# Kernel tuning notes

Measured on AMD Instinct MI355X. Metric: run time of the kernel, lower is better.

## Reference

```python
import jax, jax.numpy as jnp
import numpy as np

N = 50000
E = 800000
F_IN = 128
HID = 128
N_CLS = 32


def setup_inputs() -> dict:
    key = jax.random.key(0)
    ks = jax.random.split(key, 8)
    x = jax.random.normal(ks[0], (N, F_IN), dtype=jnp.float32)
    edge_index = jax.random.randint(ks[1], (2, E), 0, N, dtype=jnp.int32)
    batch = jnp.zeros((N,), dtype=jnp.int32)
    # GCNConv learned params (glorot-ish scale)
    W1 = jax.random.normal(ks[2], (F_IN, HID), dtype=jnp.float32) / np.sqrt(F_IN)
    b1 = jnp.zeros((HID,), dtype=jnp.float32)
    W2 = jax.random.normal(ks[3], (HID, HID), dtype=jnp.float32) / np.sqrt(HID)
    b2 = jnp.zeros((HID,), dtype=jnp.float32)
    W3 = jax.random.normal(ks[4], (HID, N_CLS), dtype=jnp.float32) / np.sqrt(HID)
    b3 = jnp.zeros((N_CLS,), dtype=jnp.float32)
    return {"x": x, "edge_index": edge_index, "batch": batch,
            "W1": W1, "b1": b1, "W2": W2, "b2": b2, "W3": W3, "b3": b3}


def _gcn_norm(edge_index, num_nodes):
    """Add self-loops and compute symmetric D^-1/2 (A+I) D^-1/2 edge weights."""
    loop = jnp.arange(num_nodes, dtype=edge_index.dtype)
    row = jnp.concatenate([edge_index[0], loop])  # source
    col = jnp.concatenate([edge_index[1], loop])  # destination
    ones = jnp.ones(row.shape[0], dtype=jnp.float32)
    deg = jax.ops.segment_sum(ones, col, num_segments=num_nodes)
    dinv = jnp.where(deg > 0, jax.lax.rsqrt(deg), 0.0)
    norm = dinv[row] * dinv[col]  # [E + N]
    return row, col, norm


def _gcn_conv(x, row, col, norm, W, b):
    h = x @ W                               # [N, out]
    msg = h[row] * norm[:, None]            # gather + scale, [E+N, out]
    out = jax.ops.segment_sum(msg, col, num_segments=x.shape[0])
    return out + b


def reference(x, edge_index, batch, W1, b1, W2, b2, W3, b3):
    # eval mode: dropout(p=0.2) is identity
    num_nodes = x.shape[0]
    row, col, norm = _gcn_norm(edge_index, num_nodes)
    h = jax.nn.relu(_gcn_conv(x, row, col, norm, W1, b1))
    h = jax.nn.relu(_gcn_conv(h, row, col, norm, W2, b2))
    out = _gcn_conv(h, row, col, norm, W3, b3)
    return out
```

## Files before the change

kernel.cpp:

```cpp
#include <hip/hip_runtime.h>
#include <math.h>


__global__ void count_kernel(const int* __restrict__ col, int* __restrict__ deg, int E, int n) {
    int e = blockIdx.x * blockDim.x + threadIdx.x;
    if (e < E) {
        int c = col[e];
        if ((unsigned)c < (unsigned)n) atomicAdd(&deg[c], 1);
    }
}

__global__ __launch_bounds__(256) void scan1_kernel(const int* __restrict__ deg,
                                                    int* __restrict__ local,
                                                    int* __restrict__ blocksums, int n) {
    __shared__ int wsum[4];
    const int t = threadIdx.x;
    const int lane = t & 63;
    const int wv = t >> 6;
    const int base = blockIdx.x * 1024 + t * 4;
    int a0 = (base + 0 < n) ? deg[base + 0] : 0;
    int a1 = (base + 1 < n) ? deg[base + 1] : 0;
    int a2 = (base + 2 < n) ? deg[base + 2] : 0;
    int a3 = (base + 3 < n) ? deg[base + 3] : 0;
    const int tot = a0 + a1 + a2 + a3;
    int incl = tot;
#pragma unroll
    for (int off = 1; off < 64; off <<= 1) {
        int u = __shfl_up(incl, off);
        if (lane >= off) incl += u;
    }
    if (lane == 63) wsum[wv] = incl;
    __syncthreads();
    int woff = 0;
#pragma unroll
    for (int w = 0; w < 4; ++w) woff += (w < wv) ? wsum[w] : 0;
    const int excl = woff + incl - tot;
    if (base + 0 < n) local[base + 0] = excl;
    if (base + 1 < n) local[base + 1] = excl + a0;
    if (base + 2 < n) local[base + 2] = excl + a0 + a1;
    if (base + 3 < n) local[base + 3] = excl + a0 + a1 + a2;
    if (t == 255) blocksums[blockIdx.x] = woff + incl;
}

__global__ void scan2_kernel(const int* __restrict__ blocksums, int* __restrict__ blockoff,
                             int* __restrict__ rowptr, int nb, int n) {
    const int lane = threadIdx.x;
    int v = (lane < nb) ? blocksums[lane] : 0;
    int incl = v;
#pragma unroll
    for (int off = 1; off < 64; off <<= 1) {
        int u = __shfl_up(incl, off);
        if (lane >= off) incl += u;
    }
    if (lane < nb) blockoff[lane] = incl - v;
    if (lane == 63) rowptr[n] = incl;
}

__global__ void scan3_kernel(const int* __restrict__ local, const int* __restrict__ blockoff,
                             const int* __restrict__ deg, int* __restrict__ rowptr,
                             int* __restrict__ cursor, float* __restrict__ dinv, int n) {
    int i = blockIdx.x * blockDim.x + threadIdx.x;
    if (i < n) {
        const int v = local[i] + blockoff[i >> 10];
        rowptr[i] = v;
        cursor[i] = v;
        dinv[i] = rsqrtf((float)deg[i] + 1.0f);
    }
}

__global__ void fill_kernel(const int* __restrict__ row, const int* __restrict__ col,
                            int* __restrict__ cursor, int* __restrict__ csr, int E, int n) {
    int e = blockIdx.x * blockDim.x + threadIdx.x;
    if (e < E) {
        int c = col[e];
        int r = row[e];
        if ((unsigned)c < (unsigned)n && (unsigned)r < (unsigned)n) {
            int pos = atomicAdd(&cursor[c], 1);
            csr[pos] = r;
        }
    }
}

template <int OUT>
__global__ __launch_bounds__(256) void gemm_kernel(const float* __restrict__ X,
                                                   const float* __restrict__ W,
                                                   const float* __restrict__ dinv,
                                                   float* __restrict__ out, int n) {
    __shared__ float Wl[128 * OUT];
    const int t = threadIdx.x;
    for (int i = t; i < 128 * OUT; i += 256) Wl[i] = W[i];
    __syncthreads();

    constexpr int CQ  = OUT / 4;
    constexpr int RG  = 256 / CQ;
    constexpr int R   = 4;
    constexpr int RPI = RG * R;
    const int cq = t % CQ;
    const int rg = t / CQ;
    const float4* X4 = (const float4*)X;

    for (int base = blockIdx.x * RPI; base < n; base += gridDim.x * RPI) {
        const int r0 = base + rg * R;
        float4 acc[R];
#pragma unroll
        for (int r = 0; r < R; ++r) acc[r] = make_float4(0.f, 0.f, 0.f, 0.f);

        if (r0 + R <= n) {
#pragma unroll 4
            for (int k4 = 0; k4 < 32; ++k4) {
                const float* wp = &Wl[k4 * 4 * OUT + cq * 4];
                float4 w0 = *(const float4*)(wp);
                float4 w1 = *(const float4*)(wp + OUT);
                float4 w2 = *(const float4*)(wp + 2 * OUT);
                float4 w3 = *(const float4*)(wp + 3 * OUT);
#pragma unroll
                for (int r = 0; r < R; ++r) {
                    float4 xv = X4[(size_t)(r0 + r) * 32 + k4];
                    acc[r].x = fmaf(xv.x, w0.x, acc[r].x);
                    acc[r].x = fmaf(xv.y, w1.x, acc[r].x);
                    acc[r].x = fmaf(xv.z, w2.x, acc[r].x);
                    acc[r].x = fmaf(xv.w, w3.x, acc[r].x);
                    acc[r].y = fmaf(xv.x, w0.y, acc[r].y);
                    acc[r].y = fmaf(xv.y, w1.y, acc[r].y);
                    acc[r].y = fmaf(xv.z, w2.y, acc[r].y);
                    acc[r].y = fmaf(xv.w, w3.y, acc[r].y);
                    acc[r].z = fmaf(xv.x, w0.z, acc[r].z);
                    acc[r].z = fmaf(xv.y, w1.z, acc[r].z);
                    acc[r].z = fmaf(xv.z, w2.z, acc[r].z);
                    acc[r].z = fmaf(xv.w, w3.z, acc[r].z);
                    acc[r].w = fmaf(xv.x, w0.w, acc[r].w);
                    acc[r].w = fmaf(xv.y, w1.w, acc[r].w);
                    acc[r].w = fmaf(xv.z, w2.w, acc[r].w);
                    acc[r].w = fmaf(xv.w, w3.w, acc[r].w);
                }
            }
#pragma unroll
            for (int r = 0; r < R; ++r) {
                const float s = dinv[r0 + r];
                acc[r].x *= s; acc[r].y *= s; acc[r].z *= s; acc[r].w *= s;
                *(float4*)&out[(size_t)(r0 + r) * OUT + cq * 4] = acc[r];
            }
        } else if (r0 < n) {
            for (int r = 0; r < R; ++r) {
                const int row = r0 + r;
                if (row >= n) break;
                float4 a = make_float4(0.f, 0.f, 0.f, 0.f);
                for (int k4 = 0; k4 < 32; ++k4) {
                    float4 xv = X4[(size_t)row * 32 + k4];
                    const float* wp = &Wl[k4 * 4 * OUT + cq * 4];
                    float4 w0 = *(const float4*)(wp);
                    float4 w1 = *(const float4*)(wp + OUT);
                    float4 w2 = *(const float4*)(wp + 2 * OUT);
                    float4 w3 = *(const float4*)(wp + 3 * OUT);
                    a.x = fmaf(xv.x, w0.x, a.x); a.x = fmaf(xv.y, w1.x, a.x);
                    a.x = fmaf(xv.z, w2.x, a.x); a.x = fmaf(xv.w, w3.x, a.x);
                    a.y = fmaf(xv.x, w0.y, a.y); a.y = fmaf(xv.y, w1.y, a.y);
                    a.y = fmaf(xv.z, w2.y, a.y); a.y = fmaf(xv.w, w3.y, a.y);
                    a.z = fmaf(xv.x, w0.z, a.z); a.z = fmaf(xv.y, w1.z, a.z);
                    a.z = fmaf(xv.z, w2.z, a.z); a.z = fmaf(xv.w, w3.z, a.z);
                    a.w = fmaf(xv.x, w0.w, a.w); a.w = fmaf(xv.y, w1.w, a.w);
                    a.w = fmaf(xv.z, w2.w, a.w); a.w = fmaf(xv.w, w3.w, a.w);
                }
                const float s = dinv[row];
                a.x *= s; a.y *= s; a.z *= s; a.w *= s;
                *(float4*)&out[(size_t)row * OUT + cq * 4] = a;
            }
        }
    }
}

template <int F, bool RELU>
__global__ __launch_bounds__(256) void agg_kernel(const float* __restrict__ hs,
                                                  const int* __restrict__ rowptr,
                                                  const int* __restrict__ csr,
                                                  const float* __restrict__ dinv,
                                                  const float* __restrict__ bias,
                                                  float* __restrict__ out, int n) {
    constexpr int LPN = F / 2;
    constexpr int NPB = 256 / LPN;
    constexpr int F2  = F / 2;
    const int t = threadIdx.x;
    const int node = blockIdx.x * NPB + t / LPN;
    const int fo = t % LPN;
    if (node >= n) return;

    const float2* h2 = (const float2*)hs;
    float2 a0 = h2[(size_t)node * F2 + fo];
    float2 a1 = {0.f, 0.f}, a2 = {0.f, 0.f}, a3 = {0.f, 0.f};
    const int s = rowptr[node];
    const int e = rowptr[node + 1];
    int i = s;
    for (; i + 4 <= e; i += 4) {
        const int r0 = csr[i + 0];
        const int r1 = csr[i + 1];
        const int r2 = csr[i + 2];
        const int r3 = csr[i + 3];
        float2 v0 = h2[(size_t)r0 * F2 + fo];
        float2 v1 = h2[(size_t)r1 * F2 + fo];
        float2 v2 = h2[(size_t)r2 * F2 + fo];
        float2 v3 = h2[(size_t)r3 * F2 + fo];
        a0.x += v0.x; a0.y += v0.y;
        a1.x += v1.x; a1.y += v1.y;
        a2.x += v2.x; a2.y += v2.y;
        a3.x += v3.x; a3.y += v3.y;
    }
    for (; i < e; ++i) {
        const int r = csr[i];
        float2 v = h2[(size_t)r * F2 + fo];
        a0.x += v.x; a0.y += v.y;
    }
    const float accx = (a0.x + a1.x) + (a2.x + a3.x);
    const float accy = (a0.y + a1.y) + (a2.y + a3.y);
    const float dc = dinv[node];
    const float2 b = *(const float2*)&bias[fo * 2];
    float ox = fmaf(accx, dc, b.x);
    float oy = fmaf(accy, dc, b.y);
    if (RELU) {
        ox = fmaxf(ox, 0.f);
        oy = fmaxf(oy, 0.f);
    }
    float2 res = {ox, oy};
    *(float2*)&out[(size_t)node * F + fo * 2] = res;
}

extern "C" void kernel_launch(void* const* d_in, const int* in_sizes, int n_in,
                              void* d_out, int out_size, void* d_ws, size_t ws_size,
                              hipStream_t stream) {
    const float* x  = (const float*)d_in[0];
    const int*   ei = (const int*)d_in[1];
    const float* W1 = (const float*)d_in[3];
    const float* b1 = (const float*)d_in[4];
    const float* W2 = (const float*)d_in[5];
    const float* b2 = (const float*)d_in[6];
    const float* W3 = (const float*)d_in[7];
    const float* b3 = (const float*)d_in[8];
    float* out = (float*)d_out;

    const int N = in_sizes[0] / 128;
    const int E = in_sizes[1] / 2;
    const int* erow = ei;
    const int* ecol = ei + E;

    char* ws = (char*)d_ws;
    auto alloc = [&](size_t bytes) {
        char* p = ws;
        ws += (bytes + 255) & ~(size_t)255;
        return p;
    };
    int*   deg    = (int*)alloc((size_t)N * 4);
    int*   rowptr = (int*)alloc((size_t)(N + 1) * 4);
    int*   cursor = (int*)alloc((size_t)N * 4);
    int*   csr    = (int*)alloc((size_t)E * 4);
    float* dinv   = (float*)alloc((size_t)N * 4);
    float* buf1   = (float*)alloc((size_t)N * 128 * 4);
    float* buf2   = (float*)alloc((size_t)N * 128 * 4);

    int* local = (int*)buf1;
    int* bsums = local + N;
    int* boffs = bsums + 64;

    const int nb = (N + 1023) / 1024;

    hipMemsetAsync(deg, 0, (size_t)N * 4, stream);
    count_kernel<<<(E + 255) / 256, 256, 0, stream>>>(ecol, deg, E, N);
    scan1_kernel<<<nb, 256, 0, stream>>>(deg, local, bsums, N);
    scan2_kernel<<<1, 64, 0, stream>>>(bsums, boffs, rowptr, nb, N);
    scan3_kernel<<<(N + 255) / 256, 256, 0, stream>>>(local, boffs, deg, rowptr, cursor, dinv, N);
    fill_kernel<<<(E + 255) / 256, 256, 0, stream>>>(erow, ecol, cursor, csr, E, N);

    gemm_kernel<128><<<512, 256, 0, stream>>>(x, W1, dinv, buf1, N);
    agg_kernel<128, true><<<(N + 3) / 4, 256, 0, stream>>>(buf1, rowptr, csr, dinv, b1, buf2, N);

    gemm_kernel<128><<<512, 256, 0, stream>>>(buf2, W2, dinv, buf1, N);
    agg_kernel<128, true><<<(N + 3) / 4, 256, 0, stream>>>(buf1, rowptr, csr, dinv, b2, buf2, N);

    gemm_kernel<32><<<512, 256, 0, stream>>>(buf2, W3, dinv, buf1, N);
    agg_kernel<32, false><<<(N + 15) / 16, 256, 0, stream>>>(buf1, rowptr, csr, dinv, b3, out, N);
}
```

Measured before the change: 319.8 us.

## Store GEMM output in feature-chunked layout and aggregate per 16-column slice

The GEMM now writes its output as column slices of 16 features each (chunk-major, node-minor), so each slice of the feature table is a compact N×16 array. A new aggregation kernel interleaves blocks across slices (blockIdx & 7 selects the slice), so concurrently running blocks gather from a smaller working set that should fit better in L2/MALL. It also adds nontemporal loads for the CSR indices and nontemporal stores for the output. In exchange, each thread gathers scalars instead of float2, and the CSR index stream is re-read once per slice.

```diff
diff --git a/kernel.cpp b/kernel.cpp
--- a/kernel.cpp
+++ b/kernel.cpp
@@ -98,6 +98,7 @@
     const int cq = t % CQ;
     const int rg = t / CQ;
     const float4* X4 = (const float4*)X;
+    const size_t chunk_off = (size_t)(cq >> 2) * n * 16 + (cq & 3) * 4;
 
     for (int base = blockIdx.x * RPI; base < n; base += gridDim.x * RPI) {
         const int r0 = base + rg * R;
@@ -138,7 +139,7 @@
             for (int r = 0; r < R; ++r) {
                 const float s = dinv[r0 + r];
                 acc[r].x *= s; acc[r].y *= s; acc[r].z *= s; acc[r].w *= s;
-                *(float4*)&out[(size_t)(r0 + r) * OUT + cq * 4] = acc[r];
+                *(float4*)&out[chunk_off + (size_t)(r0 + r) * 16] = acc[r];
             }
         } else if (r0 < n) {
             for (int r = 0; r < R; ++r) {
@@ -163,64 +164,55 @@
                 }
                 const float s = dinv[row];
                 a.x *= s; a.y *= s; a.z *= s; a.w *= s;
-                *(float4*)&out[(size_t)row * OUT + cq * 4] = a;
+                *(float4*)&out[chunk_off + (size_t)row * 16] = a;
             }
         }
     }
 }
 
-template <int F, bool RELU>
-__global__ __launch_bounds__(256) void agg_kernel(const float* __restrict__ hs,
-                                                  const int* __restrict__ rowptr,
-                                                  const int* __restrict__ csr,
-                                                  const float* __restrict__ dinv,
-                                                  const float* __restrict__ bias,
-                                                  float* __restrict__ out, int n) {
-    constexpr int LPN = F / 2;
-    constexpr int NPB = 256 / LPN;
-    constexpr int F2  = F / 2;
+template <int NC, bool RELU>
+__global__ __launch_bounds__(256) void agg_chunk_kernel(const float* __restrict__ hc,
+                                                        const int* __restrict__ rowptr,
+                                                        const int* __restrict__ csr,
+                                                        const float* __restrict__ dinv,
+                                                        const float* __restrict__ bias,
+                                                        float* __restrict__ out, int n) {
+    constexpr int F = NC * 16;
+    constexpr int NSPLIT = 8 / NC;
     const int t = threadIdx.x;
-    const int node = blockIdx.x * NPB + t / LPN;
-    const int fo = t % LPN;
+    const int slot = blockIdx.x & 7;
+    const int cc = slot % NC;
+    const int split = slot / NC;
+    const int g = (blockIdx.x >> 3) * NSPLIT + split;
+    const int node = g * 16 + (t >> 4);
+    const int ln = t & 15;
     if (node >= n) return;
 
-    const float2* h2 = (const float2*)hs;
-    float2 a0 = h2[(size_t)node * F2 + fo];
-    float2 a1 = {0.f, 0.f}, a2 = {0.f, 0.f}, a3 = {0.f, 0.f};
+    const float* __restrict__ slice = hc + (size_t)cc * n * 16;
+    float a0 = slice[(size_t)node * 16 + ln];
+    float a1 = 0.f, a2 = 0.f, a3 = 0.f;
     const int s = rowptr[node];
     const int e = rowptr[node + 1];
     int i = s;
     for (; i + 4 <= e; i += 4) {
-        const int r0 = csr[i + 0];
-        const int r1 = csr[i + 1];
-        const int r2 = csr[i + 2];
-        const int r3 = csr[i + 3];
-        float2 v0 = h2[(size_t)r0 * F2 + fo];
-        float2 v1 = h2[(size_t)r1 * F2 + fo];
-        float2 v2 = h2[(size_t)r2 * F2 + fo];
-        float2 v3 = h2[(size_t)r3 * F2 + fo];
-        a0.x += v0.x; a0.y += v0.y;
-        a1.x += v1.x; a1.y += v1.y;
-        a2.x += v2.x; a2.y += v2.y;
-        a3.x += v3.x; a3.y += v3.y;
+        const int r0 = __builtin_nontemporal_load(&csr[i + 0]);
+        const int r1 = __builtin_nontemporal_load(&csr[i + 1]);
+        const int r2 = __builtin_nontemporal_load(&csr[i + 2]);
+        const int r3 = __builtin_nontemporal_load(&csr[i + 3]);
+        a0 += slice[(size_t)r0 * 16 + ln];
+        a1 += slice[(size_t)r1 * 16 + ln];
+        a2 += slice[(size_t)r2 * 16 + ln];
+        a3 += slice[(size_t)r3 * 16 + ln];
     }
     for (; i < e; ++i) {
-        const int r = csr[i];
-        float2 v = h2[(size_t)r * F2 + fo];
-        a0.x += v.x; a0.y += v.y;
-    }
-    const float accx = (a0.x + a1.x) + (a2.x + a3.x);
-    const float accy = (a0.y + a1.y) + (a2.y + a3.y);
-    const float dc = dinv[node];
-    const float2 b = *(const float2*)&bias[fo * 2];
-    float ox = fmaf(accx, dc, b.x);
-    float oy = fmaf(accy, dc, b.y);
-    if (RELU) {
-        ox = fmaxf(ox, 0.f);
-        oy = fmaxf(oy, 0.f);
-    }
-    float2 res = {ox, oy};
-    *(float2*)&out[(size_t)node * F + fo * 2] = res;
+        const int r = __builtin_nontemporal_load(&csr[i]);
+        a0 += slice[(size_t)r * 16 + ln];
+    }
+    const float acc = (a0 + a1) + (a2 + a3);
+    const int f = cc * 16 + ln;
+    float o = fmaf(acc, dinv[node], bias[f]);
+    if (RELU) o = fmaxf(o, 0.f);
+    __builtin_nontemporal_store(o, &out[(size_t)node * F + f]);
 }
 
 extern "C" void kernel_launch(void* const* d_in, const int* in_sizes, int n_in,
@@ -268,12 +260,16 @@
     scan3_kernel<<<(N + 255) / 256, 256, 0, stream>>>(local, boffs, deg, rowptr, cursor, dinv, N);
     fill_kernel<<<(E + 255) / 256, 256, 0, stream>>>(erow, ecol, cursor, csr, E, N);
 
+    const int ngroups = (N + 15) / 16;
+    const int grid128 = ngroups * 8;
+    const int grid32  = ((ngroups + 3) / 4) * 8;
+
     gemm_kernel<128><<<512, 256, 0, stream>>>(x, W1, dinv, buf1, N);
-    agg_kernel<128, true><<<(N + 3) / 4, 256, 0, stream>>>(buf1, rowptr, csr, dinv, b1, buf2, N);
+    agg_chunk_kernel<8, true><<<grid128, 256, 0, stream>>>(buf1, rowptr, csr, dinv, b1, buf2, N);
 
     gemm_kernel<128><<<512, 256, 0, stream>>>(buf2, W2, dinv, buf1, N);
-    agg_kernel<128, true><<<(N + 3) / 4, 256, 0, stream>>>(buf1, rowptr, csr, dinv, b2, buf2, N);
+    agg_chunk_kernel<8, true><<<grid128, 256, 0, stream>>>(buf1, rowptr, csr, dinv, b2, buf2, N);
 
     gemm_kernel<32><<<512, 256, 0, stream>>>(buf2, W3, dinv, buf1, N);
-    agg_kernel<32, false><<<(N + 15) / 16, 256, 0, stream>>>(buf1, rowptr, csr, dinv, b3, out, N);
-}
+    agg_chunk_kernel<2, false><<<grid32, 256, 0, stream>>>(buf1, rowptr, csr, dinv, b3, out, N);
+}
```

Result: slower. 442.6 us (+38.4%).
